# Optimization experiments

Hardware: AMD Instinct MI355X
Metric: run time of the kernel (lower is better)

The kernel has to match this reference:

```python
import jax, jax.numpy as jnp
import numpy as np

N_NODES = 100000
N_EDGES = 1600000


def setup_inputs() -> dict:
    key = jax.random.key(0)
    ks = jax.random.split(key, 8)
    s = 0.1  # small init scale
    return {
        "x": jax.random.normal(ks[0], (N_NODES, 58), jnp.float32),
        "edge_index": jax.random.randint(ks[1], (2, N_EDGES), 0, N_NODES, dtype=jnp.int32),
        "Wi1": s * jax.random.normal(ks[2], (2, 58, 16), jnp.float32),
        "Wr1": s * jax.random.normal(ks[3], (2, 58, 16), jnp.float32),
        "b1": s * jax.random.normal(ks[4], (2, 16), jnp.float32),
        "Wi2": s * jax.random.normal(ks[5], (2, 16, 1), jnp.float32),
        "Wr2": s * jax.random.normal(ks[6], (2, 16, 1), jnp.float32),
        "b2": s * jax.random.normal(ks[7], (2, 1), jnp.float32),
    }


def _gcn_norm(edge_index, n_nodes):
    # PyG gcn_norm with add_self_loops=False: deg from target col, sym norm
    row, col = edge_index[0], edge_index[1]
    deg = jax.ops.segment_sum(jnp.ones((edge_index.shape[1],), jnp.float32), col,
                              num_segments=n_nodes)
    dis = jnp.where(deg > 0, jax.lax.rsqrt(jnp.maximum(deg, 1.0)), 0.0)
    return row, col, dis[row] * dis[col]  # per-edge norm


def _arma_layer(x, row, col, norm, Wi, Wr, b, n_nodes):
    # T=1, shared_weights, eval-mode (internal dropout off):
    # out_k = relu(A_hat @ (x @ Wi_k) + x @ Wr_k + b_k); mean over K stacks
    h = jnp.einsum('nf,kfo->kno', x, Wi)          # [K, N, F_out]
    msg = h[:, row, :] * norm[None, :, None]      # [K, E, F_out]
    agg = jax.vmap(lambda m: jax.ops.segment_sum(m, col, num_segments=n_nodes))(msg)
    root = jnp.einsum('nf,kfo->kno', x, Wr)       # [K, N, F_out]
    return jax.nn.relu(agg + root + b[:, None, :]).mean(axis=0)


def reference(x, edge_index, Wi1, Wr1, b1, Wi2, Wr2, b2):
    row, col, norm = _gcn_norm(edge_index, N_NODES)
    h = _arma_layer(x, row, col, norm, Wi1, Wr1, b1, N_NODES)  # conv1 (relu inside)
    h = jax.nn.relu(h)                                         # wrapper F.relu
    # F.dropout(p=0.5) is identity in eval mode
    out = _arma_layer(h, row, col, norm, Wi2, Wr2, b2, N_NODES)  # conv2
    return out  # [N, 1]
```

## Files before the change

kernel.cpp:

```cpp
#include <hip/hip_runtime.h>

#define NN 100000
#define NE 1600000

constexpr int F_IN = 58;
constexpr int FH2  = 32;
constexpr int KS   = 2;

constexpr int NB   = 391;
constexpr int NBLK = 256;
constexpr int EPB  = NE / NBLK;
constexpr int SCANN = NB * NBLK;
constexpr int SCAN_BLOCKS = (SCANN + 1023) / 1024;
constexpr int DN_NODES = 64;
constexpr int DENSE_BLOCKS = (NN + DN_NODES - 1) / DN_NODES;
constexpr int LROW = 136;

using short8 = __attribute__((ext_vector_type(8))) short;
using f32x4  = __attribute__((ext_vector_type(4))) float;

__device__ inline void splitbf(float v, short& hi, short& lo) {
    unsigned ub = __float_as_uint(v);
    unsigned short h = (unsigned short)(ub >> 16);
    float hif = __uint_as_float(((unsigned)h) << 16);
    float lof = v - hif;
    unsigned short l = (unsigned short)(__float_as_uint(lof) >> 16);
    hi = (short)h; lo = (short)l;
}

__global__ void k_prep_w(const float* __restrict__ Wi, const float* __restrict__ Wr,
                         short* __restrict__ wpre) {
    int t = threadIdx.x;
    for (int idx = t; idx < 64 * 64; idx += 256) {
        int c = idx >> 6, i = idx & 63;
        int ko = c & 31, kst = ko >> 4, o = ko & 15;
        const float* W = (c < 32) ? Wi : Wr;
        float v = (i < F_IN) ? W[(kst * F_IN + i) * 16 + o] : 0.f;
        short hi, lo; splitbf(v, hi, lo);
        wpre[c * 128 + i] = hi;
        wpre[c * 128 + 64 + i] = lo;
    }
}

__global__ void k_hist_dense1(const int* __restrict__ col, int* __restrict__ bh,
                              const float* __restrict__ x,
                              const short* __restrict__ wpre,
                              const float* __restrict__ b,
                              float* __restrict__ h1, float* __restrict__ r1) {
    __shared__ int hist[NB];
    __shared__ short sA[64 * LROW];
    __shared__ short sB[64 * LROW];
    int tid = threadIdx.x;

    if (blockIdx.x < NBLK) {
        int blk = blockIdx.x;
        for (int i = tid; i < NB; i += 256) hist[i] = 0;
        __syncthreads();
        const int2* c2p = (const int2*)&col[blk * EPB];
        for (int c = tid; c < EPB / 2; c += 256) {
            int2 cc = c2p[c];
            atomicAdd(&hist[cc.x >> 8], 1);
            atomicAdd(&hist[cc.y >> 8], 1);
        }
        __syncthreads();
        for (int i = tid; i < NB; i += 256)
            bh[i * NBLK + blk] = hist[i];
        return;
    }

    int nodeBase = (blockIdx.x - NBLK) * DN_NODES;
    for (int t = tid; t < 1024; t += 256) {
        int c = t >> 4, q8 = t & 15;
        *(short8*)&sB[c * LROW + q8 * 8] = *(const short8*)&wpre[c * 128 + q8 * 8];
    }
    for (int t = tid; t < 1024; t += 256) {
        int r = t >> 4, q4 = t & 15;
        int n = nodeBase + r;
        float v0 = 0.f, v1 = 0.f, v2 = 0.f, v3 = 0.f;
        int i0 = q4 * 4;
        if (n < NN && i0 < F_IN) {
            float2 a = *(const float2*)&x[(size_t)n * F_IN + i0];
            v0 = a.x; v1 = a.y;
            if (i0 + 2 < F_IN) {
                float2 c2 = *(const float2*)&x[(size_t)n * F_IN + i0 + 2];
                v2 = c2.x; v3 = c2.y;
            }
        }
        short h0, l0, h1s, l1s, h2s, l2s, h3s, l3s;
        splitbf(v0, h0, l0); splitbf(v1, h1s, l1s);
        splitbf(v2, h2s, l2s); splitbf(v3, h3s, l3s);
        *(short4*)&sA[r * LROW + q4 * 4]      = make_short4(h0, h1s, h2s, h3s);
        *(short4*)&sA[r * LROW + 64 + q4 * 4] = make_short4(l0, l1s, l2s, l3s);
    }
    __syncthreads();

    int lane = tid & 63, w = tid >> 6;
    int r15 = lane & 15, h4 = lane >> 4;
    const short* aB = &sA[(w * 16 + r15) * LROW];
    f32x4 acc0 = {0,0,0,0}, acc1 = {0,0,0,0}, acc2 = {0,0,0,0}, acc3 = {0,0,0,0};
    const int kaA[6] = {0, 32, 0, 32, 64, 96};
    const int kaB[6] = {0, 32, 64, 96, 0, 32};
#pragma unroll
    for (int s = 0; s < 6; s++) {
        short8 af = *(const short8*)&aB[kaA[s] + h4 * 8];
#define BMM(nt, accv) { \
        short8 bf = *(const short8*)&sB[(nt * 16 + r15) * LROW + kaB[s] + h4 * 8]; \
        accv = __builtin_amdgcn_mfma_f32_16x16x32_bf16(af, bf, accv, 0, 0, 0); }
        BMM(0, acc0) BMM(1, acc1) BMM(2, acc2) BMM(3, acc3)
#undef BMM
    }
    int nb0 = nodeBase + w * 16 + h4 * 4;
#define WH(nt, accv) { int colg = nt * 16 + r15; \
    if (nb0 + 0 < NN) h1[(size_t)(nb0 + 0) * 32 + colg] = accv[0]; \
    if (nb0 + 1 < NN) h1[(size_t)(nb0 + 1) * 32 + colg] = accv[1]; \
    if (nb0 + 2 < NN) h1[(size_t)(nb0 + 2) * 32 + colg] = accv[2]; \
    if (nb0 + 3 < NN) h1[(size_t)(nb0 + 3) * 32 + colg] = accv[3]; }
#define WR(nt, accv) { int colg = nt * 16 + r15 - 32; float bv = b[colg]; \
    if (nb0 + 0 < NN) r1[(size_t)(nb0 + 0) * 32 + colg] = accv[0] + bv; \
    if (nb0 + 1 < NN) r1[(size_t)(nb0 + 1) * 32 + colg] = accv[1] + bv; \
    if (nb0 + 2 < NN) r1[(size_t)(nb0 + 2) * 32 + colg] = accv[2] + bv; \
    if (nb0 + 3 < NN) r1[(size_t)(nb0 + 3) * 32 + colg] = accv[3] + bv; }
    WH(0, acc0) WH(1, acc1) WR(2, acc2) WR(3, acc3)
#undef WH
#undef WR
}

__global__ void k_scan1(int* __restrict__ bh, int* __restrict__ bsum) {
    __shared__ int ts[256];
    int tid = threadIdx.x;
    int base = blockIdx.x * 1024 + tid * 4;
    int v0 = (base + 0 < SCANN) ? bh[base + 0] : 0;
    int v1 = (base + 1 < SCANN) ? bh[base + 1] : 0;
    int v2 = (base + 2 < SCANN) ? bh[base + 2] : 0;
    int v3 = (base + 3 < SCANN) ? bh[base + 3] : 0;
    int p0 = v0, p1 = p0 + v1, p2 = p1 + v2, p3 = p2 + v3;
    ts[tid] = p3;
    __syncthreads();
    for (int off = 1; off < 256; off <<= 1) {
        int v = (tid >= off) ? ts[tid - off] : 0;
        __syncthreads();
        ts[tid] += v;
        __syncthreads();
    }
    int prev = (tid > 0) ? ts[tid - 1] : 0;
    if (base + 0 < SCANN) bh[base + 0] = prev + p0;
    if (base + 1 < SCANN) bh[base + 1] = prev + p1;
    if (base + 2 < SCANN) bh[base + 2] = prev + p2;
    if (base + 3 < SCANN) bh[base + 3] = prev + p3;
    if (tid == 255) bsum[blockIdx.x] = ts[255];
}

__global__ void k_scan2(const int* __restrict__ bsum, int* __restrict__ boff) {
    __shared__ int s[128];
    int tid = threadIdx.x;
    s[tid] = (tid < SCAN_BLOCKS) ? bsum[tid] : 0;
    __syncthreads();
    for (int off = 1; off < 128; off <<= 1) {
        int v = (tid >= off) ? s[tid - off] : 0;
        __syncthreads();
        s[tid] += v;
        __syncthreads();
    }
    if (tid < SCAN_BLOCKS) boff[tid] = (tid > 0) ? s[tid - 1] : 0;
}

__global__ void k_bscatter(const int* __restrict__ row, const int* __restrict__ col,
                           const int* __restrict__ bh, const int* __restrict__ boff,
                           int* __restrict__ ebuck) {
    __shared__ int cur[NB];
    int tid = threadIdx.x, blk = blockIdx.x;
    for (int i = tid; i < NB; i += 256) {
        int idx = i * NBLK + blk;
        cur[i] = (idx == 0) ? 0 : bh[idx - 1] + boff[(idx - 1) >> 10];
    }
    __syncthreads();
    int base = blk * EPB;
    const int2* c2p = (const int2*)&col[base];
    const int2* r2p = (const int2*)&row[base];
    for (int c = tid; c < EPB / 2; c += 256) {
        int2 cc = c2p[c];
        int2 rr = r2p[c];
        int p0 = atomicAdd(&cur[cc.x >> 8], 1);
        ebuck[p0] = (rr.x << 8) | (cc.x & 255);
        int p1 = atomicAdd(&cur[cc.y >> 8], 1);
        ebuck[p1] = (rr.y << 8) | (cc.y & 255);
    }
}

__global__ void __launch_bounds__(256) k_bcsr_a(const int* __restrict__ bh,
                                                const int* __restrict__ boff,
                                                const int* __restrict__ ebuck,
                                                int* __restrict__ inc, float* __restrict__ dis) {
    __shared__ int cnt[514];
    __shared__ int scn[256];
    int b = blockIdx.x, tid = threadIdx.x;
    int i0 = b * NBLK - 1, i1 = (b + 1) * NBLK - 1;
    int start = (b == 0) ? 0 : bh[i0] + boff[i0 >> 10];
    int end   = bh[i1] + boff[i1 >> 10];
    cnt[tid] = 0; cnt[257 + tid] = 0;
    __syncthreads();
    int c0 = (tid & 1) * 257;
    for (int j = start + tid; j < end; j += 256)
        atomicAdd(&cnt[c0 + (ebuck[j] & 255)], 1);
    __syncthreads();
    int v = cnt[tid] + cnt[257 + tid];
    scn[tid] = v;
    __syncthreads();
    for (int off = 1; off < 256; off <<= 1) {
        int t = (tid >= off) ? scn[tid - off] : 0;
        __syncthreads();
        scn[tid] += t;
        __syncthreads();
    }
    int colIdx = (b << 8) + tid;
    if (colIdx < NN) {
        inc[colIdx] = start + scn[tid];
        dis[colIdx] = (v > 0) ? rsqrtf((float)v) : 0.f;
    }
}

__global__ void __launch_bounds__(256) k_bcsr_b(const int* __restrict__ bh,
                                                const int* __restrict__ boff,
                                                const int* __restrict__ ebuck,
                                                const int* __restrict__ inc,
                                                const float* __restrict__ dis,
                                                int2* __restrict__ esrc8) {
    __shared__ int cur[256];
    __shared__ float sdis[256];
    int b = blockIdx.x, tid = threadIdx.x;
    int i0 = b * NBLK - 1, i1 = (b + 1) * NBLK - 1;
    int start = (b == 0) ? 0 : bh[i0] + boff[i0 >> 10];
    int end   = bh[i1] + boff[i1 >> 10];
    int colIdx = (b << 8) + tid;
    cur[tid]  = (colIdx == 0) ? 0 : ((colIdx <= NN) ? inc[colIdx - 1] : 0);
    sdis[tid] = (colIdx < NN) ? dis[colIdx] : 0.f;
    __syncthreads();
    for (int j = start + tid; j < end; j += 256) {
        int e = ebuck[j];
        int c = e & 255, s = e >> 8;
        int pos = atomicAdd(&cur[c], 1);
        float w = dis[s] * sdis[c];
        esrc8[pos] = make_int2(s, __float_as_int(w));
    }
}

__global__ void k_gather1_mid(const int* __restrict__ inc, const int2* __restrict__ esrc8,
                              const float4* __restrict__ h1, const float4* __restrict__ r1,
                              const float4* __restrict__ Wi2, const float4* __restrict__ Wr2,
                              const float* __restrict__ b2,
                              float* __restrict__ h2, float* __restrict__ r2) {
    int tid = blockIdx.x * blockDim.x + threadIdx.x;
    int n = tid >> 3, l = tid & 7;
    if (n >= NN) return;
    int js = (n == 0) ? 0 : inc[n - 1];
    int je = inc[n];
    float4 acc = r1[(size_t)n * 8 + l];
    int j = js;
    if ((j & 1) && j < je) {
        int2 e = esrc8[j];
        float w = __int_as_float(e.y);
        float4 v = h1[(size_t)e.x * 8 + l];
        acc.x = fmaf(w, v.x, acc.x); acc.y = fmaf(w, v.y, acc.y);
        acc.z = fmaf(w, v.z, acc.z); acc.w = fmaf(w, v.w, acc.w);
        j++;
    }
    for (; j + 1 < je; j += 2) {
        int4 ep = *(const int4*)&esrc8[j];
        float w0 = __int_as_float(ep.y), w1 = __int_as_float(ep.w);
        float4 v0 = h1[(size_t)ep.x * 8 + l];
        float4 v1 = h1[(size_t)ep.z * 8 + l];
        acc.x = fmaf(w0, v0.x, acc.x); acc.y = fmaf(w0, v0.y, acc.y);
        acc.z = fmaf(w0, v0.z, acc.z); acc.w = fmaf(w0, v0.w, acc.w);
        acc.x = fmaf(w1, v1.x, acc.x); acc.y = fmaf(w1, v1.y, acc.y);
        acc.z = fmaf(w1, v1.z, acc.z); acc.w = fmaf(w1, v1.w, acc.w);
    }
    if (j < je) {
        int2 e = esrc8[j];
        float w = __int_as_float(e.y);
        float4 v = h1[(size_t)e.x * 8 + l];
        acc.x = fmaf(w, v.x, acc.x); acc.y = fmaf(w, v.y, acc.y);
        acc.z = fmaf(w, v.z, acc.z); acc.w = fmaf(w, v.w, acc.w);
    }
    acc.x = fmaxf(acc.x, 0.f); acc.y = fmaxf(acc.y, 0.f);
    acc.z = fmaxf(acc.z, 0.f); acc.w = fmaxf(acc.w, 0.f);
    float4 h;
    h.x = 0.5f * (acc.x + __shfl_xor(acc.x, 4));
    h.y = 0.5f * (acc.y + __shfl_xor(acc.y, 4));
    h.z = 0.5f * (acc.z + __shfl_xor(acc.z, 4));
    h.w = 0.5f * (acc.w + __shfl_xor(acc.w, 4));
    float4 wi = Wi2[l], wr = Wr2[l];
    float p1 = h.x * wi.x + h.y * wi.y + h.z * wi.z + h.w * wi.w;
    float p2 = h.x * wr.x + h.y * wr.y + h.z * wr.z + h.w * wr.w;
    p1 += __shfl_xor(p1, 1); p1 += __shfl_xor(p1, 2);
    p2 += __shfl_xor(p2, 1); p2 += __shfl_xor(p2, 2);
    if ((l & 3) == 0) {
        int k = l >> 2;
        h2[n * 2 + k] = p1;
        r2[n * 2 + k] = p2 + b2[k];
    }
}

__global__ void k_gather2(const int* __restrict__ inc, const int2* __restrict__ esrc8,
                          const float* __restrict__ h2, const float* __restrict__ r2,
                          float* __restrict__ out) {
    int tid = blockIdx.x * blockDim.x + threadIdx.x;
    int n = tid >> 3, l = tid & 7;
    if (n >= NN) return;
    int js = (n == 0) ? 0 : inc[n - 1];
    int je = inc[n];
    float a0 = 0.f, a1v = 0.f;
    for (int j = js + l; j < je; j += 8) {
        int2 e = esrc8[j];
        float w = __int_as_float(e.y);
        float2 hv = *(const float2*)&h2[(size_t)e.x * 2];
        a0  = fmaf(w, hv.x, a0);
        a1v = fmaf(w, hv.y, a1v);
    }
    a0  += __shfl_xor(a0, 1);  a0  += __shfl_xor(a0, 2);  a0  += __shfl_xor(a0, 4);
    a1v += __shfl_xor(a1v, 1); a1v += __shfl_xor(a1v, 2); a1v += __shfl_xor(a1v, 4);
    if (l == 0) {
        float2 rv = *(const float2*)&r2[(size_t)n * 2];
        out[n] = 0.5f * (fmaxf(a0 + rv.x, 0.f) + fmaxf(a1v + rv.y, 0.f));
    }
}

extern "C" void kernel_launch(void* const* d_in, const int* in_sizes, int n_in,
                              void* d_out, int out_size, void* d_ws, size_t ws_size,
                              hipStream_t stream) {
    const float* x   = (const float*)d_in[0];
    const int*   ei  = (const int*)d_in[1];
    const float* Wi1 = (const float*)d_in[2];
    const float* Wr1 = (const float*)d_in[3];
    const float* b1  = (const float*)d_in[4];
    const float* Wi2 = (const float*)d_in[5];
    const float* Wr2 = (const float*)d_in[6];
    const float* b2  = (const float*)d_in[7];
    float* out = (float*)d_out;

    const int* row = ei;
    const int* col = ei + NE;

    int*   bh    = (int*)d_ws;
    int*   bsum  = bh + SCANN;
    int*   boff  = bsum + 128;
    float* dis   = (float*)(boff + 128);
    int*   inc   = (int*)(dis + NN);
    short* wpre  = (short*)(inc + NN);
    int*   ebuck = (int*)(wpre + 8192);
    int2*  esrc8 = (int2*)(ebuck + NE);
    float* h1    = (float*)(esrc8 + NE);
    float* r1    = h1 + (size_t)NN * FH2;
    float* h2    = r1 + (size_t)NN * FH2;
    float* r2    = h2 + (size_t)NN * KS;

    const int B = 256;
    k_prep_w<<<1, B, 0, stream>>>(Wi1, Wr1, wpre);
    k_hist_dense1<<<NBLK + DENSE_BLOCKS, B, 0, stream>>>(col, bh, x, wpre, b1, h1, r1);
    k_scan1<<<SCAN_BLOCKS, B, 0, stream>>>(bh, bsum);
    k_scan2<<<1, 128, 0, stream>>>(bsum, boff);
    k_bscatter<<<NBLK, B, 0, stream>>>(row, col, bh, boff, ebuck);
    k_bcsr_a<<<NB, B, 0, stream>>>(bh, boff, ebuck, inc, dis);
    k_bcsr_b<<<NB, B, 0, stream>>>(bh, boff, ebuck, inc, dis, esrc8);
    k_gather1_mid<<<(NN * 8 + B - 1) / B, B, 0, stream>>>(inc, esrc8,
        (const float4*)h1, (const float4*)r1, (const float4*)Wi2, (const float4*)Wr2,
        b2, h2, r2);
    k_gather2<<<(NN * 8 + B - 1) / B, B, 0, stream>>>(inc, esrc8, h2, r2, out);
}
```

Baseline: 111.6 us.

## Halve bucket width to 128 columns, unroll gather1 by four, narrow gather2 lanes

```diff
diff --git a/kernel.cpp b/kernel.cpp
--- a/kernel.cpp
+++ b/kernel.cpp
@@ -7,7 +7,7 @@
 constexpr int FH2  = 32;
 constexpr int KS   = 2;
 
-constexpr int NB   = 391;
+constexpr int NB   = 782;
 constexpr int NBLK = 256;
 constexpr int EPB  = NE / NBLK;
 constexpr int SCANN = NB * NBLK;
@@ -59,8 +59,8 @@
         const int2* c2p = (const int2*)&col[blk * EPB];
         for (int c = tid; c < EPB / 2; c += 256) {
             int2 cc = c2p[c];
-            atomicAdd(&hist[cc.x >> 8], 1);
-            atomicAdd(&hist[cc.y >> 8], 1);
+            atomicAdd(&hist[cc.x >> 7], 1);
+            atomicAdd(&hist[cc.y >> 7], 1);
         }
         __syncthreads();
         for (int i = tid; i < NB; i += 256)
@@ -151,11 +151,11 @@
 }
 
 __global__ void k_scan2(const int* __restrict__ bsum, int* __restrict__ boff) {
-    __shared__ int s[128];
+    __shared__ int s[256];
     int tid = threadIdx.x;
     s[tid] = (tid < SCAN_BLOCKS) ? bsum[tid] : 0;
     __syncthreads();
-    for (int off = 1; off < 128; off <<= 1) {
+    for (int off = 1; off < 256; off <<= 1) {
         int v = (tid >= off) ? s[tid - off] : 0;
         __syncthreads();
         s[tid] += v;
@@ -180,10 +180,10 @@
     for (int c = tid; c < EPB / 2; c += 256) {
         int2 cc = c2p[c];
         int2 rr = r2p[c];
-        int p0 = atomicAdd(&cur[cc.x >> 8], 1);
-        ebuck[p0] = (rr.x << 8) | (cc.x & 255);
-        int p1 = atomicAdd(&cur[cc.y >> 8], 1);
-        ebuck[p1] = (rr.y << 8) | (cc.y & 255);
+        int p0 = atomicAdd(&cur[cc.x >> 7], 1);
+        ebuck[p0] = (rr.x << 7) | (cc.x & 127);
+        int p1 = atomicAdd(&cur[cc.y >> 7], 1);
+        ebuck[p1] = (rr.y << 7) | (cc.y & 127);
     }
 }
 
@@ -191,31 +191,33 @@
                                                 const int* __restrict__ boff,
                                                 const int* __restrict__ ebuck,
                                                 int* __restrict__ inc, float* __restrict__ dis) {
-    __shared__ int cnt[514];
-    __shared__ int scn[256];
+    __shared__ int cnt[258];
+    __shared__ int scn[128];
     int b = blockIdx.x, tid = threadIdx.x;
     int i0 = b * NBLK - 1, i1 = (b + 1) * NBLK - 1;
     int start = (b == 0) ? 0 : bh[i0] + boff[i0 >> 10];
     int end   = bh[i1] + boff[i1 >> 10];
-    cnt[tid] = 0; cnt[257 + tid] = 0;
-    __syncthreads();
-    int c0 = (tid & 1) * 257;
+    if (tid < 129) { cnt[tid] = 0; cnt[129 + tid] = 0; }
+    __syncthreads();
+    int c0 = (tid & 1) * 129;
     for (int j = start + tid; j < end; j += 256)
-        atomicAdd(&cnt[c0 + (ebuck[j] & 255)], 1);
-    __syncthreads();
-    int v = cnt[tid] + cnt[257 + tid];
-    scn[tid] = v;
-    __syncthreads();
-    for (int off = 1; off < 256; off <<= 1) {
-        int t = (tid >= off) ? scn[tid - off] : 0;
-        __syncthreads();
-        scn[tid] += t;
-        __syncthreads();
-    }
-    int colIdx = (b << 8) + tid;
-    if (colIdx < NN) {
-        inc[colIdx] = start + scn[tid];
-        dis[colIdx] = (v > 0) ? rsqrtf((float)v) : 0.f;
+        atomicAdd(&cnt[c0 + (ebuck[j] & 127)], 1);
+    __syncthreads();
+    int v = 0;
+    if (tid < 128) { v = cnt[tid] + cnt[129 + tid]; scn[tid] = v; }
+    __syncthreads();
+    for (int off = 1; off < 128; off <<= 1) {
+        int t = (tid < 128 && tid >= off) ? scn[tid - off] : 0;
+        __syncthreads();
+        if (tid < 128) scn[tid] += t;
+        __syncthreads();
+    }
+    if (tid < 128) {
+        int colIdx = (b << 7) + tid;
+        if (colIdx < NN) {
+            inc[colIdx] = start + scn[tid];
+            dis[colIdx] = (v > 0) ? rsqrtf((float)v) : 0.f;
+        }
     }
 }
 
@@ -225,19 +227,21 @@
                                                 const int* __restrict__ inc,
                                                 const float* __restrict__ dis,
                                                 int2* __restrict__ esrc8) {
-    __shared__ int cur[256];
-    __shared__ float sdis[256];
+    __shared__ int cur[128];
+    __shared__ float sdis[128];
     int b = blockIdx.x, tid = threadIdx.x;
     int i0 = b * NBLK - 1, i1 = (b + 1) * NBLK - 1;
     int start = (b == 0) ? 0 : bh[i0] + boff[i0 >> 10];
     int end   = bh[i1] + boff[i1 >> 10];
-    int colIdx = (b << 8) + tid;
-    cur[tid]  = (colIdx == 0) ? 0 : ((colIdx <= NN) ? inc[colIdx - 1] : 0);
-    sdis[tid] = (colIdx < NN) ? dis[colIdx] : 0.f;
+    if (tid < 128) {
+        int colIdx = (b << 7) + tid;
+        cur[tid]  = (colIdx == 0) ? 0 : ((colIdx <= NN) ? inc[colIdx - 1] : 0);
+        sdis[tid] = (colIdx < NN) ? dis[colIdx] : 0.f;
+    }
     __syncthreads();
     for (int j = start + tid; j < end; j += 256) {
         int e = ebuck[j];
-        int c = e & 255, s = e >> 8;
+        int c = e & 127, s = e >> 7;
         int pos = atomicAdd(&cur[c], 1);
         float w = dis[s] * sdis[c];
         esrc8[pos] = make_int2(s, __float_as_int(w));
@@ -256,31 +260,33 @@
     int je = inc[n];
     float4 acc = r1[(size_t)n * 8 + l];
     int j = js;
+#define EDGE1(ss, ww) { \
+        float4 v = h1[(size_t)(ss) * 8 + l]; \
+        acc.x = fmaf(ww, v.x, acc.x); acc.y = fmaf(ww, v.y, acc.y); \
+        acc.z = fmaf(ww, v.z, acc.z); acc.w = fmaf(ww, v.w, acc.w); }
     if ((j & 1) && j < je) {
         int2 e = esrc8[j];
-        float w = __int_as_float(e.y);
-        float4 v = h1[(size_t)e.x * 8 + l];
-        acc.x = fmaf(w, v.x, acc.x); acc.y = fmaf(w, v.y, acc.y);
-        acc.z = fmaf(w, v.z, acc.z); acc.w = fmaf(w, v.w, acc.w);
+        EDGE1(e.x, __int_as_float(e.y))
         j++;
+    }
+    for (; j + 3 < je; j += 4) {
+        int4 ep0 = *(const int4*)&esrc8[j];
+        int4 ep1 = *(const int4*)&esrc8[j + 2];
+        EDGE1(ep0.x, __int_as_float(ep0.y))
+        EDGE1(ep0.z, __int_as_float(ep0.w))
+        EDGE1(ep1.x, __int_as_float(ep1.y))
+        EDGE1(ep1.z, __int_as_float(ep1.w))
     }
     for (; j + 1 < je; j += 2) {
         int4 ep = *(const int4*)&esrc8[j];
-        float w0 = __int_as_float(ep.y), w1 = __int_as_float(ep.w);
-        float4 v0 = h1[(size_t)ep.x * 8 + l];
-        float4 v1 = h1[(size_t)ep.z * 8 + l];
-        acc.x = fmaf(w0, v0.x, acc.x); acc.y = fmaf(w0, v0.y, acc.y);
-        acc.z = fmaf(w0, v0.z, acc.z); acc.w = fmaf(w0, v0.w, acc.w);
-        acc.x = fmaf(w1, v1.x, acc.x); acc.y = fmaf(w1, v1.y, acc.y);
-        acc.z = fmaf(w1, v1.z, acc.z); acc.w = fmaf(w1, v1.w, acc.w);
+        EDGE1(ep.x, __int_as_float(ep.y))
+        EDGE1(ep.z, __int_as_float(ep.w))
     }
     if (j < je) {
         int2 e = esrc8[j];
-        float w = __int_as_float(e.y);
-        float4 v = h1[(size_t)e.x * 8 + l];
-        acc.x = fmaf(w, v.x, acc.x); acc.y = fmaf(w, v.y, acc.y);
-        acc.z = fmaf(w, v.z, acc.z); acc.w = fmaf(w, v.w, acc.w);
-    }
+        EDGE1(e.x, __int_as_float(e.y))
+    }
+#undef EDGE1
     acc.x = fmaxf(acc.x, 0.f); acc.y = fmaxf(acc.y, 0.f);
     acc.z = fmaxf(acc.z, 0.f); acc.w = fmaxf(acc.w, 0.f);
     float4 h;
@@ -304,20 +310,20 @@
                           const float* __restrict__ h2, const float* __restrict__ r2,
                           float* __restrict__ out) {
     int tid = blockIdx.x * blockDim.x + threadIdx.x;
-    int n = tid >> 3, l = tid & 7;
+    int n = tid >> 2, l = tid & 3;
     if (n >= NN) return;
     int js = (n == 0) ? 0 : inc[n - 1];
     int je = inc[n];
     float a0 = 0.f, a1v = 0.f;
-    for (int j = js + l; j < je; j += 8) {
+    for (int j = js + l; j < je; j += 4) {
         int2 e = esrc8[j];
         float w = __int_as_float(e.y);
         float2 hv = *(const float2*)&h2[(size_t)e.x * 2];
         a0  = fmaf(w, hv.x, a0);
         a1v = fmaf(w, hv.y, a1v);
     }
-    a0  += __shfl_xor(a0, 1);  a0  += __shfl_xor(a0, 2);  a0  += __shfl_xor(a0, 4);
-    a1v += __shfl_xor(a1v, 1); a1v += __shfl_xor(a1v, 2); a1v += __shfl_xor(a1v, 4);
+    a0  += __shfl_xor(a0, 1);  a0  += __shfl_xor(a0, 2);
+    a1v += __shfl_xor(a1v, 1); a1v += __shfl_xor(a1v, 2);
     if (l == 0) {
         float2 rv = *(const float2*)&r2[(size_t)n * 2];
         out[n] = 0.5f * (fmaxf(a0 + rv.x, 0.f) + fmaxf(a1v + rv.y, 0.f));
@@ -342,8 +348,8 @@
 
     int*   bh    = (int*)d_ws;
     int*   bsum  = bh + SCANN;
-    int*   boff  = bsum + 128;
-    float* dis   = (float*)(boff + 128);
+    int*   boff  = bsum + 256;
+    float* dis   = (float*)(boff + 256);
     int*   inc   = (int*)(dis + NN);
     short* wpre  = (short*)(inc + NN);
     int*   ebuck = (int*)(wpre + 8192);
@@ -357,12 +363,12 @@
     k_prep_w<<<1, B, 0, stream>>>(Wi1, Wr1, wpre);
     k_hist_dense1<<<NBLK + DENSE_BLOCKS, B, 0, stream>>>(col, bh, x, wpre, b1, h1, r1);
     k_scan1<<<SCAN_BLOCKS, B, 0, stream>>>(bh, bsum);
-    k_scan2<<<1, 128, 0, stream>>>(bsum, boff);
+    k_scan2<<<1, 256, 0, stream>>>(bsum, boff);
     k_bscatter<<<NBLK, B, 0, stream>>>(row, col, bh, boff, ebuck);
     k_bcsr_a<<<NB, B, 0, stream>>>(bh, boff, ebuck, inc, dis);
     k_bcsr_b<<<NB, B, 0, stream>>>(bh, boff, ebuck, inc, dis, esrc8);
     k_gather1_mid<<<(NN * 8 + B - 1) / B, B, 0, stream>>>(inc, esrc8,
         (const float4*)h1, (const float4*)r1, (const float4*)Wi2, (const float4*)Wr2,
         b2, h2, r2);
-    k_gather2<<<(NN * 8 + B - 1) / B, B, 0, stream>>>(inc, esrc8, h2, r2, out);
-}
+    k_gather2<<<(NN * 4 + B - 1) / B, B, 0, stream>>>(inc, esrc8, h2, r2, out);
+}
```

Result: no change. 112.2 us (+0.5%).

## Fuse CSR build kernels and compute edge weights on the fly in gathers

Applied to the files above, without the earlier changes.

```diff
diff --git a/kernel.cpp b/kernel.cpp
--- a/kernel.cpp
+++ b/kernel.cpp
@@ -187,12 +187,14 @@
     }
 }
 
-__global__ void __launch_bounds__(256) k_bcsr_a(const int* __restrict__ bh,
-                                                const int* __restrict__ boff,
-                                                const int* __restrict__ ebuck,
-                                                int* __restrict__ inc, float* __restrict__ dis) {
+__global__ void __launch_bounds__(256) k_bcsr(const int* __restrict__ bh,
+                                              const int* __restrict__ boff,
+                                              const int* __restrict__ ebuck,
+                                              int* __restrict__ inc, float* __restrict__ dis,
+                                              int* __restrict__ esrc) {
     __shared__ int cnt[514];
     __shared__ int scn[256];
+    __shared__ int cur[256];
     int b = blockIdx.x, tid = threadIdx.x;
     int i0 = b * NBLK - 1, i1 = (b + 1) * NBLK - 1;
     int start = (b == 0) ? 0 : bh[i0] + boff[i0 >> 10];
@@ -212,39 +214,23 @@
         scn[tid] += t;
         __syncthreads();
     }
+    int incl = scn[tid];
+    cur[tid] = start + incl - v;
     int colIdx = (b << 8) + tid;
     if (colIdx < NN) {
-        inc[colIdx] = start + scn[tid];
+        inc[colIdx] = start + incl;
         dis[colIdx] = (v > 0) ? rsqrtf((float)v) : 0.f;
     }
-}
-
-__global__ void __launch_bounds__(256) k_bcsr_b(const int* __restrict__ bh,
-                                                const int* __restrict__ boff,
-                                                const int* __restrict__ ebuck,
-                                                const int* __restrict__ inc,
-                                                const float* __restrict__ dis,
-                                                int2* __restrict__ esrc8) {
-    __shared__ int cur[256];
-    __shared__ float sdis[256];
-    int b = blockIdx.x, tid = threadIdx.x;
-    int i0 = b * NBLK - 1, i1 = (b + 1) * NBLK - 1;
-    int start = (b == 0) ? 0 : bh[i0] + boff[i0 >> 10];
-    int end   = bh[i1] + boff[i1 >> 10];
-    int colIdx = (b << 8) + tid;
-    cur[tid]  = (colIdx == 0) ? 0 : ((colIdx <= NN) ? inc[colIdx - 1] : 0);
-    sdis[tid] = (colIdx < NN) ? dis[colIdx] : 0.f;
     __syncthreads();
     for (int j = start + tid; j < end; j += 256) {
         int e = ebuck[j];
-        int c = e & 255, s = e >> 8;
-        int pos = atomicAdd(&cur[c], 1);
-        float w = dis[s] * sdis[c];
-        esrc8[pos] = make_int2(s, __float_as_int(w));
-    }
-}
-
-__global__ void k_gather1_mid(const int* __restrict__ inc, const int2* __restrict__ esrc8,
+        int pos = atomicAdd(&cur[e & 255], 1);
+        esrc[pos] = e >> 8;
+    }
+}
+
+__global__ void k_gather1_mid(const int* __restrict__ inc, const int* __restrict__ esrc,
+                              const float* __restrict__ dis,
                               const float4* __restrict__ h1, const float4* __restrict__ r1,
                               const float4* __restrict__ Wi2, const float4* __restrict__ Wr2,
                               const float* __restrict__ b2,
@@ -254,33 +240,21 @@
     if (n >= NN) return;
     int js = (n == 0) ? 0 : inc[n - 1];
     int je = inc[n];
+    float dn = dis[n];
     float4 acc = r1[(size_t)n * 8 + l];
     int j = js;
-    if ((j & 1) && j < je) {
-        int2 e = esrc8[j];
-        float w = __int_as_float(e.y);
-        float4 v = h1[(size_t)e.x * 8 + l];
-        acc.x = fmaf(w, v.x, acc.x); acc.y = fmaf(w, v.y, acc.y);
-        acc.z = fmaf(w, v.z, acc.z); acc.w = fmaf(w, v.w, acc.w);
-        j++;
-    }
-    for (; j + 1 < je; j += 2) {
-        int4 ep = *(const int4*)&esrc8[j];
-        float w0 = __int_as_float(ep.y), w1 = __int_as_float(ep.w);
-        float4 v0 = h1[(size_t)ep.x * 8 + l];
-        float4 v1 = h1[(size_t)ep.z * 8 + l];
-        acc.x = fmaf(w0, v0.x, acc.x); acc.y = fmaf(w0, v0.y, acc.y);
-        acc.z = fmaf(w0, v0.z, acc.z); acc.w = fmaf(w0, v0.w, acc.w);
-        acc.x = fmaf(w1, v1.x, acc.x); acc.y = fmaf(w1, v1.y, acc.y);
-        acc.z = fmaf(w1, v1.z, acc.z); acc.w = fmaf(w1, v1.w, acc.w);
-    }
-    if (j < je) {
-        int2 e = esrc8[j];
-        float w = __int_as_float(e.y);
-        float4 v = h1[(size_t)e.x * 8 + l];
-        acc.x = fmaf(w, v.x, acc.x); acc.y = fmaf(w, v.y, acc.y);
-        acc.z = fmaf(w, v.z, acc.z); acc.w = fmaf(w, v.w, acc.w);
-    }
+#define EDGE1(ss) { \
+        float w = dis[ss] * dn; \
+        float4 v = h1[(size_t)(ss) * 8 + l]; \
+        acc.x = fmaf(w, v.x, acc.x); acc.y = fmaf(w, v.y, acc.y); \
+        acc.z = fmaf(w, v.z, acc.z); acc.w = fmaf(w, v.w, acc.w); }
+    while (j < je && (j & 3)) { EDGE1(esrc[j]) j++; }
+    for (; j + 3 < je; j += 4) {
+        int4 s4 = *(const int4*)&esrc[j];
+        EDGE1(s4.x) EDGE1(s4.y) EDGE1(s4.z) EDGE1(s4.w)
+    }
+    for (; j < je; j++) { EDGE1(esrc[j]) }
+#undef EDGE1
     acc.x = fmaxf(acc.x, 0.f); acc.y = fmaxf(acc.y, 0.f);
     acc.z = fmaxf(acc.z, 0.f); acc.w = fmaxf(acc.w, 0.f);
     float4 h;
@@ -300,7 +274,8 @@
     }
 }
 
-__global__ void k_gather2(const int* __restrict__ inc, const int2* __restrict__ esrc8,
+__global__ void k_gather2(const int* __restrict__ inc, const int* __restrict__ esrc,
+                          const float* __restrict__ dis,
                           const float* __restrict__ h2, const float* __restrict__ r2,
                           float* __restrict__ out) {
     int tid = blockIdx.x * blockDim.x + threadIdx.x;
@@ -308,11 +283,12 @@
     if (n >= NN) return;
     int js = (n == 0) ? 0 : inc[n - 1];
     int je = inc[n];
+    float dn = dis[n];
     float a0 = 0.f, a1v = 0.f;
     for (int j = js + l; j < je; j += 8) {
-        int2 e = esrc8[j];
-        float w = __int_as_float(e.y);
-        float2 hv = *(const float2*)&h2[(size_t)e.x * 2];
+        int s = esrc[j];
+        float w = dis[s] * dn;
+        float2 hv = *(const float2*)&h2[(size_t)s * 2];
         a0  = fmaf(w, hv.x, a0);
         a1v = fmaf(w, hv.y, a1v);
     }
@@ -347,8 +323,8 @@
     int*   inc   = (int*)(dis + NN);
     short* wpre  = (short*)(inc + NN);
     int*   ebuck = (int*)(wpre + 8192);
-    int2*  esrc8 = (int2*)(ebuck + NE);
-    float* h1    = (float*)(esrc8 + NE);
+    int*   esrc  = ebuck + NE;
+    float* h1    = (float*)(esrc + NE);
     float* r1    = h1 + (size_t)NN * FH2;
     float* h2    = r1 + (size_t)NN * FH2;
     float* r2    = h2 + (size_t)NN * KS;
@@ -359,10 +335,9 @@
     k_scan1<<<SCAN_BLOCKS, B, 0, stream>>>(bh, bsum);
     k_scan2<<<1, 128, 0, stream>>>(bsum, boff);
     k_bscatter<<<NBLK, B, 0, stream>>>(row, col, bh, boff, ebuck);
-    k_bcsr_a<<<NB, B, 0, stream>>>(bh, boff, ebuck, inc, dis);
-    k_bcsr_b<<<NB, B, 0, stream>>>(bh, boff, ebuck, inc, dis, esrc8);
-    k_gather1_mid<<<(NN * 8 + B - 1) / B, B, 0, stream>>>(inc, esrc8,
+    k_bcsr<<<NB, B, 0, stream>>>(bh, boff, ebuck, inc, dis, esrc);
+    k_gather1_mid<<<(NN * 8 + B - 1) / B, B, 0, stream>>>(inc, esrc, dis,
         (const float4*)h1, (const float4*)r1, (const float4*)Wi2, (const float4*)Wr2,
         b2, h2, r2);
-    k_gather2<<<(NN * 8 + B - 1) / B, B, 0, stream>>>(inc, esrc8, h2, r2, out);
-}
+    k_gather2<<<(NN * 8 + B - 1) / B, B, 0, stream>>>(inc, esrc, dis, h2, r2, out);
+}
```

New measurement: 106.5 us. 1.05x faster.
